# Kernel optimization log

Measured on AMD Instinct MI355X. Metric: run time of the kernel, lower is better.

The kernel has to match this reference:

```python
import jax, jax.numpy as jnp
import numpy as np

D_MODEL = 2048
N_HEADS = 16
HEAD_DIM = D_MODEL // N_HEADS


def setup_inputs() -> dict:
    key = jax.random.key(0)
    k_x, k_wqkv, k_bqkv, k_wo, k_bo = jax.random.split(key, 5)
    B, T = 4, 1024
    s_in = 1.0 / np.sqrt(D_MODEL)
    return {
        "x": jax.random.normal(k_x, (B, T, D_MODEL), dtype=jnp.float32),
        "w_qkv": jax.random.uniform(k_wqkv, (D_MODEL, 3 * D_MODEL), jnp.float32, -s_in, s_in),
        "b_qkv": jax.random.uniform(k_bqkv, (3 * D_MODEL,), jnp.float32, -s_in, s_in),
        "w_out": jax.random.uniform(k_wo, (D_MODEL, D_MODEL), jnp.float32, -s_in, s_in),
        "b_out": jax.random.uniform(k_bo, (D_MODEL,), jnp.float32, -s_in, s_in),
    }


def reference(x, w_qkv, b_qkv, w_out, b_out) -> jnp.ndarray:
    B, T, C = x.shape
    qkv = x @ w_qkv + b_qkv                      # [B, T, 3C]
    q, k, v = jnp.split(qkv, 3, axis=-1)
    # [B, H, T, Dh]
    q = q.reshape(B, T, N_HEADS, HEAD_DIM).transpose(0, 2, 1, 3)
    k = k.reshape(B, T, N_HEADS, HEAD_DIM).transpose(0, 2, 1, 3)
    v = v.reshape(B, T, N_HEADS, HEAD_DIM).transpose(0, 2, 1, 3)
    scale = 1.0 / np.sqrt(HEAD_DIM).astype(np.float32)
    att = jnp.einsum("bhqd,bhkd->bhqk", q, k) * scale   # [B, H, T, T]
    causal = jnp.tril(jnp.ones((T, T), dtype=bool))
    att = jnp.where(causal, att, -jnp.inf)
    att = jax.nn.softmax(att, axis=-1)
    out = jnp.einsum("bhqk,bhkd->bhqd", att, v)          # [B, H, T, Dh]
    out = out.transpose(0, 2, 1, 3).reshape(B, T, C)
    return out @ w_out + b_out
```

## Files before the change

kernel.cpp:

```cpp
#include <hip/hip_runtime.h>
#include <hip/hip_bf16.h>
#include <math.h>

#define DM    2048
#define DQKV  6144
#define NH    16
#define DH    128
#define TT    1024
#define BB    4

typedef __bf16 bf16_t;
typedef __bf16 bf16x4 __attribute__((ext_vector_type(4)));
typedef __bf16 bf16x8 __attribute__((ext_vector_type(8)));
typedef float  f32x4  __attribute__((ext_vector_type(4)));

__device__ __forceinline__ void async16(const void* g, void* lds) {
  __builtin_amdgcn_global_load_lds(
      (const __attribute__((address_space(1))) unsigned int*)g,
      (__attribute__((address_space(3))) unsigned int*)lds, 16, 0, 0);
}

__device__ __forceinline__ void block_barrier() {
  asm volatile("" ::: "memory");
  __builtin_amdgcn_s_barrier();
  asm volatile("" ::: "memory");
}

__global__ __launch_bounds__(256) void prep_kernel(
    const float* __restrict__ x, bf16_t* __restrict__ xb,
    const float* __restrict__ w_qkv, bf16_t* __restrict__ wqkv_t,
    const float* __restrict__ w_out, bf16_t* __restrict__ wout_t) {
  const int tid = threadIdx.x;
  const int bx = blockIdx.x;
  if (bx < 4096) {
    const size_t i = ((size_t)bx * 256 + tid) * 8;
    float4 a = *(const float4*)(x + i);
    float4 b = *(const float4*)(x + i + 4);
    bf16x8 o = {(bf16_t)a.x, (bf16_t)a.y, (bf16_t)a.z, (bf16_t)a.w,
                (bf16_t)b.x, (bf16_t)b.y, (bf16_t)b.z, (bf16_t)b.w};
    *(bf16x8*)(xb + i) = o;
    return;
  }
  __shared__ bf16_t tile[64][72];
  const float* W;
  bf16_t* Wt;
  int K, N, tn, tk;
  if (bx < 7168) {
    const int t = bx - 4096;
    W = w_qkv; Wt = wqkv_t; K = 2048; N = 6144;
    tn = (t % 96) * 64; tk = (t / 96) * 64;
  } else {
    const int t = bx - 7168;
    W = w_out; Wt = wout_t; K = 2048; N = 2048;
    tn = (t % 32) * 64; tk = (t / 32) * 64;
  }
  {
    int r = tid >> 2, c0 = (tid & 3) * 16;
    const float* src = W + (size_t)(tk + r) * N + tn + c0;
#pragma unroll
    for (int j = 0; j < 4; ++j) {
      float4 v = *(const float4*)(src + j * 4);
      tile[r][c0 + j * 4 + 0] = (bf16_t)v.x;
      tile[r][c0 + j * 4 + 1] = (bf16_t)v.y;
      tile[r][c0 + j * 4 + 2] = (bf16_t)v.z;
      tile[r][c0 + j * 4 + 3] = (bf16_t)v.w;
    }
  }
  __syncthreads();
  {
    int n = tid >> 2, c0 = (tid & 3) * 16;
    bf16_t* dst = Wt + (size_t)(tn + n) * K + tk + c0;
#pragma unroll
    for (int j = 0; j < 4; ++j) {
      bf16x4 t = {tile[c0 + j * 4 + 0][n], tile[c0 + j * 4 + 1][n],
                  tile[c0 + j * 4 + 2][n], tile[c0 + j * 4 + 3][n]};
      *(bf16x4*)(dst + j * 4) = t;
    }
  }
}

__global__ __launch_bounds__(256) void v_transpose_kernel(
    const bf16_t* __restrict__ qkv, bf16_t* __restrict__ Vt_g) {
  __shared__ bf16_t tile[64][72];
  const int tid = threadIdx.x;
  const int dt = blockIdx.x;
  const int tt = blockIdx.y;
  const int bh = blockIdx.z;
  const int b = bh >> 4, h = bh & 15;
  {
    int r = tid >> 2, c0 = (tid & 3) * 16;
    const bf16_t* src =
        qkv + (size_t)(b * TT + tt * 64 + r) * DQKV + 2 * DM + h * DH + dt * 64 + c0;
    *(bf16x8*)&tile[r][c0]     = *(const bf16x8*)(src);
    *(bf16x8*)&tile[r][c0 + 8] = *(const bf16x8*)(src + 8);
  }
  __syncthreads();
  {
    int n = tid >> 2, c0 = (tid & 3) * 16;
    bf16_t* dst = Vt_g + (size_t)(bh * DH + dt * 64 + n) * TT + tt * 64 + c0;
#pragma unroll
    for (int j = 0; j < 4; ++j) {
      bf16x4 t = {tile[c0 + j * 4 + 0][n], tile[c0 + j * 4 + 1][n],
                  tile[c0 + j * 4 + 2][n], tile[c0 + j * 4 + 3][n]};
      *(bf16x4*)(dst + j * 4) = t;
    }
  }
}

template <bool OUT_BF16, int BCH, bool WRITE_VT>
__global__ __launch_bounds__(512, 2) void gemm_big_kernel(
    const bf16_t* __restrict__ A, const bf16_t* __restrict__ Bt,
    const float* __restrict__ bias, void* __restrict__ out,
    bf16_t* __restrict__ vt, int M, int N, int K, int nbm) {
  __shared__ __align__(16) bf16_t As[2][256 * 64];
  __shared__ __align__(16) bf16_t Bs[2][BCH * 64 * 64];

  const int tid  = threadIdx.x;
  const int lane = tid & 63;
  const int wave = tid >> 6;
  const int ln   = lane & 15;
  const int quad = lane >> 4;

  const int cpx = gridDim.x >> 3;
  const int wg  = (blockIdx.x & 7) * cpx + (blockIdx.x >> 3);
  const int bm  = wg & (nbm - 1);
  const int bn  = wg / nbm;

  const bf16_t* Abase = A + (size_t)bm * 256 * K;
  const bf16_t* Bbase = Bt + (size_t)bn * (BCH * 64) * K;

  const int m0 = (wave >> 2) * 128;
  const int n0 = (wave & 3) * (BCH * 16);

  f32x4 acc[8][BCH] = {};

  const int NT = K >> 6;

  auto stageA = [&](int kt, int d) {
#pragma unroll
    for (int s = 0; s < 4; ++s) {
      const int fb  = s * 512 + wave * 64;
      const int f   = fb + lane;
      const int row = f >> 3, c = f & 7;
      const int gc  = c ^ (row & 7);
      async16(Abase + (size_t)row * K + kt * 64 + gc * 8,
              (char*)(&As[d][0]) + fb * 16);
    }
  };
  auto stageB = [&](int kt, int d) {
#pragma unroll
    for (int s = 0; s < BCH; ++s) {
      const int fb  = s * 512 + wave * 64;
      const int f   = fb + lane;
      const int row = f >> 3, c = f & 7;
      const int gc  = c ^ (row & 7);
      async16(Bbase + (size_t)row * K + kt * 64 + gc * 8,
              (char*)(&Bs[d][0]) + fb * 16);
    }
  };
  auto vm_lpt = [&] {
    if constexpr (BCH == 3)
      asm volatile("s_waitcnt vmcnt(7)" ::: "memory");
    else
      asm volatile("s_waitcnt vmcnt(6)" ::: "memory");
  };

  stageA(0, 0);
  stageB(0, 0);
  stageA(1, 1);
  stageB(1, 1);
  vm_lpt();
  block_barrier();

  for (int kt = 0; kt < NT; ++kt) {
    const int cur = kt & 1;

    bf16x8 af[8][2], bfr[BCH][2];
#pragma unroll
    for (int ks = 0; ks < 2; ++ks) {
#pragma unroll
      for (int i = 0; i < 8; ++i) {
        const int row = m0 + 16 * i + ln;
        const int c = (ks * 4 + quad) ^ (row & 7);
        af[i][ks] =
            *(const bf16x8*)((const char*)(&As[cur][0]) + ((row * 8 + c) << 4));
      }
#pragma unroll
      for (int j = 0; j < BCH; ++j) {
        const int row = n0 + 16 * j + ln;
        const int c = (ks * 4 + quad) ^ (row & 7);
        bfr[j][ks] =
            *(const bf16x8*)((const char*)(&Bs[cur][0]) + ((row * 8 + c) << 4));
      }
    }
    asm volatile("s_waitcnt lgkmcnt(0)" ::: "memory");
    block_barrier();

    if (kt + 2 < NT) stageA(kt + 2, cur);
    __builtin_amdgcn_s_setprio(1);
#pragma unroll
    for (int i = 0; i < 8; ++i)
#pragma unroll
      for (int j = 0; j < BCH; ++j)
        acc[i][j] = __builtin_amdgcn_mfma_f32_16x16x32_bf16(af[i][0], bfr[j][0],
                                                            acc[i][j], 0, 0, 0);
    __builtin_amdgcn_s_setprio(0);
    if (kt + 2 < NT) stageB(kt + 2, cur);
    __builtin_amdgcn_s_setprio(1);
#pragma unroll
    for (int i = 0; i < 8; ++i)
#pragma unroll
      for (int j = 0; j < BCH; ++j)
        acc[i][j] = __builtin_amdgcn_mfma_f32_16x16x32_bf16(af[i][1], bfr[j][1],
                                                            acc[i][j], 0, 0, 0);
    __builtin_amdgcn_s_setprio(0);

    if (kt + 2 < NT)
      vm_lpt();
    else
      asm volatile("s_waitcnt vmcnt(0)" ::: "memory");
    block_barrier();
  }

#pragma unroll
  for (int i = 0; i < 8; ++i) {
    const int rowg = bm * 256 + m0 + 16 * i + quad * 4;
#pragma unroll
    for (int j = 0; j < BCH; ++j) {
      const int cb   = bn * (BCH * 64) + n0 + 16 * j;
      const int colg = cb + ln;
      const float bb = bias[colg];
      if (WRITE_VT && cb >= 2 * DM) {
        const int vrow = ((rowg >> 10) << 11) + (colg - 2 * DM);
        bf16x4 v = {(bf16_t)(acc[i][j][0] + bb), (bf16_t)(acc[i][j][1] + bb),
                    (bf16_t)(acc[i][j][2] + bb), (bf16_t)(acc[i][j][3] + bb)};
        *(bf16x4*)(vt + (size_t)vrow * TT + (rowg & (TT - 1))) = v;
      } else {
#pragma unroll
        for (int r = 0; r < 4; ++r) {
          float val = acc[i][j][r] + bb;
          if (OUT_BF16)
            ((bf16_t*)out)[(size_t)(rowg + r) * N + colg] = (bf16_t)val;
          else
            ((float*)out)[(size_t)(rowg + r) * N + colg] = val;
        }
      }
    }
  }
}

__global__ __launch_bounds__(256, 2) void attn_kernel(
    const bf16_t* __restrict__ qkv, const bf16_t* __restrict__ Vt_g,
    bf16_t* __restrict__ attout) {
  const int bx = blockIdx.x;
  const int bh = bx & 63;
  const int j_  = bx >> 6;
  const int rr  = j_ >> 2, cc_ = j_ & 3;
  const int qt  = (rr & 1) ? (rr * 4 + (3 - cc_)) : (rr * 4 + cc_);
  const int b  = bh >> 4;
  const int h  = bh & 15;
  const int tid  = threadIdx.x;
  const int lane = tid & 63;
  const int wave = tid >> 6;
  const int ln   = lane & 15;
  const int quad = lane >> 4;

  __shared__ __align__(16) bf16_t Ks[2][64 * 128];
  __shared__ __align__(16) bf16_t Vs[2][128 * 64];
  __shared__ __align__(16) bf16_t Ps[4 * 16 * 64];

  const float scale = 0.08838834764831845f;
  const float SHIFT = 12.0f;
  const int q0 = qt * 64 + wave * 16;

  bf16x8 aq[4];
  {
    const bf16_t* qrow = qkv + (size_t)(b * TT + q0 + ln) * DQKV + h * DH;
#pragma unroll
    for (int kt = 0; kt < 4; ++kt)
      aq[kt] = *(const bf16x8*)(qrow + kt * 32 + quad * 8);
  }

  auto stage = [&](int c, int buf) {
    const int kc = c * 64;
#pragma unroll
    for (int j = 0; j < 4; ++j) {
      const int fb = j * 256 + wave * 64;
      const int l  = fb + lane;
      {
        const int row = l >> 4, cc = l & 15;
        const int gc  = cc ^ (row & 7);
        const bf16_t* g =
            qkv + (size_t)(b * TT + kc + row) * DQKV + DM + h * DH + gc * 8;
        async16(g, (char*)(&Ks[buf][0]) + fb * 16);
      }
      {
        const int d = l >> 3, cc = l & 7;
        const int gc = cc ^ (d & 7);
        const bf16_t* g = Vt_g + (size_t)(bh * DH + d) * TT + kc + gc * 8;
        async16(g, (char*)(&Vs[buf][0]) + fb * 16);
      }
    }
  };

  f32x4 o[8] = {};
  float lp[4] = {0.f, 0.f, 0.f, 0.f};

  stage(0, 0);

  for (int c = 0; c <= qt; ++c) {
    const int cur = c & 1;
    const char* Kc = (const char*)(&Ks[cur][0]);
    const char* Vc = (const char*)(&Vs[cur][0]);

    asm volatile("s_waitcnt lgkmcnt(0)" ::: "memory");
    block_barrier();
    if (c < qt) {
      stage(c + 1, cur ^ 1);
      asm volatile("s_waitcnt vmcnt(8)" ::: "memory");
    } else {
      asm volatile("s_waitcnt vmcnt(0)" ::: "memory");
    }
    block_barrier();

    f32x4 sacc[4];
    __builtin_amdgcn_s_setprio(1);
#pragma unroll
    for (int jt = 0; jt < 4; ++jt) {
      sacc[jt] = (f32x4){0.f, 0.f, 0.f, 0.f};
#pragma unroll
      for (int kt = 0; kt < 4; ++kt) {
        const int row = jt * 16 + ln;
        const int sc  = (kt * 4 + quad) ^ (row & 7);
        bf16x8 bk = *(const bf16x8*)(Kc + row * 256 + sc * 16);
        sacc[jt] = __builtin_amdgcn_mfma_f32_16x16x32_bf16(aq[kt], bk,
                                                           sacc[jt], 0, 0, 0);
      }
    }
    __builtin_amdgcn_s_setprio(0);

    const int kc = c * 64;
    const bool diag = (c == qt);
#pragma unroll
    for (int jt = 0; jt < 4; ++jt) {
      const int colg = kc + jt * 16 + ln;
#pragma unroll
      for (int r = 0; r < 4; ++r) {
        float sv = sacc[jt][r] * scale - SHIFT;
        if (diag && colg > q0 + quad * 4 + r) sv = -1e30f;
        float pv = __expf(sv);
        lp[r] += pv;
        const int row = quad * 4 + r;
        const int col = jt * 16 + ln;
        const int sc  = (col >> 3) ^ (row & 7);
        Ps[wave * 1024 + row * 64 + sc * 8 + (col & 7)] = (bf16_t)pv;
      }
    }

    __builtin_amdgcn_s_setprio(1);
#pragma unroll
    for (int ks = 0; ks < 2; ++ks) {
      const int psc = (ks * 4 + quad) ^ (ln & 7);
      bf16x8 ap =
          *(const bf16x8*)((const char*)Ps + wave * 2048 + ln * 128 + psc * 16);
#pragma unroll
      for (int nt = 0; nt < 8; ++nt) {
        const int row = nt * 16 + ln;
        const int sc  = (ks * 4 + quad) ^ (row & 7);
        bf16x8 bv = *(const bf16x8*)(Vc + row * 128 + sc * 16);
        o[nt] = __builtin_amdgcn_mfma_f32_16x16x32_bf16(ap, bv, o[nt], 0, 0, 0);
      }
    }
    __builtin_amdgcn_s_setprio(0);
  }

#pragma unroll
  for (int off = 1; off < 16; off <<= 1)
#pragma unroll
    for (int r = 0; r < 4; ++r) lp[r] += __shfl_xor(lp[r], off, 64);

#pragma unroll
  for (int r = 0; r < 4; ++r) {
    float inv = 1.0f / lp[r];
    int t = q0 + quad * 4 + r;
    bf16_t* orow = attout + (size_t)(b * TT + t) * DM + h * DH;
#pragma unroll
    for (int nt = 0; nt < 8; ++nt)
      orow[nt * 16 + ln] = (bf16_t)(o[nt][r] * inv);
  }
}

extern "C" void kernel_launch(void* const* d_in, const int* in_sizes, int n_in,
                              void* d_out, int out_size, void* d_ws,
                              size_t ws_size, hipStream_t stream) {
  const float* x     = (const float*)d_in[0];
  const float* w_qkv = (const float*)d_in[1];
  const float* b_qkv = (const float*)d_in[2];
  const float* w_out = (const float*)d_in[3];
  const float* b_out = (const float*)d_in[4];
  float* out = (float*)d_out;

  char* ws = (char*)d_ws;
  bf16_t* qkv    = (bf16_t*)(ws);
  bf16_t* wqkv_t = (bf16_t*)(ws + 50331648);
  bf16_t* wout_t = (bf16_t*)(ws + 75497472);
  bf16_t* xb     = (bf16_t*)(ws + 83886080);
  bf16_t* attout = xb;

  const bool fuse_vt = (ws_size >= 117440512);
  bf16_t* Vt_g = fuse_vt ? (bf16_t*)(ws + 100663296) : wqkv_t;

  prep_kernel<<<dim3(8192), dim3(256), 0, stream>>>(x, xb, w_qkv, wqkv_t,
                                                    w_out, wout_t);
  if (fuse_vt) {
    gemm_big_kernel<true, 3, true><<<dim3(512), dim3(512), 0, stream>>>(
        xb, wqkv_t, b_qkv, qkv, Vt_g, 4096, 6144, 2048, 16);
  } else {
    gemm_big_kernel<true, 3, false><<<dim3(512), dim3(512), 0, stream>>>(
        xb, wqkv_t, b_qkv, qkv, nullptr, 4096, 6144, 2048, 16);
    v_transpose_kernel<<<dim3(2, 16, 64), dim3(256), 0, stream>>>(qkv, Vt_g);
  }
  attn_kernel<<<dim3(1024), dim3(256), 0, stream>>>(qkv, Vt_g, attout);
  gemm_big_kernel<false, 2, false><<<dim3(256), dim3(512), 0, stream>>>(
      attout, wout_t, b_out, out, nullptr, 4096, 2048, 2048, 16);
}
```

Before: 329.9 us.

## Restructure GEMM main loop into quadrant-ordered MFMA phases with split A prefetch

The main loop of the bf16 GEMM now loads A and B fragments from LDS in four smaller quadrant phases instead of loading all of them up front. Each phase's MFMAs run as soon as its fragments arrive, and B fragments are reused across phases, which cuts register pressure and overlaps LDS reads with matrix math. The A tile's global-to-LDS staging is split in two. Half of the next tile is prefetched into the idle buffer while the current tile is being computed, and the other half plus B is issued after the barrier, with adjusted vmcnt waits. The aim is to hide memory latency better and lower VGPR use, at the cost of tricky wait-count accounting and more phase boundaries.

Result: slower. 361.8 us (+9.7%).

```diff
diff --git a/kernel.cpp b/kernel.cpp
--- a/kernel.cpp
+++ b/kernel.cpp
@@ -136,88 +136,134 @@
 
   const int NT = K >> 6;
 
-  auto stageA = [&](int kt, int d) {
-#pragma unroll
-    for (int s = 0; s < 4; ++s) {
-      const int fb  = s * 512 + wave * 64;
-      const int f   = fb + lane;
-      const int row = f >> 3, c = f & 7;
-      const int gc  = c ^ (row & 7);
-      async16(Abase + (size_t)row * K + kt * 64 + gc * 8,
-              (char*)(&As[d][0]) + fb * 16);
-    }
+  auto sA = [&](int kt, int d, int s) {
+    const int fb  = s * 512 + wave * 64;
+    const int f   = fb + lane;
+    const int row = f >> 3, c = f & 7;
+    const int gc  = c ^ (row & 7);
+    async16(Abase + (size_t)row * K + kt * 64 + gc * 8,
+            (char*)(&As[d][0]) + fb * 16);
   };
-  auto stageB = [&](int kt, int d) {
-#pragma unroll
-    for (int s = 0; s < BCH; ++s) {
-      const int fb  = s * 512 + wave * 64;
-      const int f   = fb + lane;
-      const int row = f >> 3, c = f & 7;
-      const int gc  = c ^ (row & 7);
-      async16(Bbase + (size_t)row * K + kt * 64 + gc * 8,
-              (char*)(&Bs[d][0]) + fb * 16);
-    }
+  auto sB = [&](int kt, int d, int s) {
+    const int fb  = s * 512 + wave * 64;
+    const int f   = fb + lane;
+    const int row = f >> 3, c = f & 7;
+    const int gc  = c ^ (row & 7);
+    async16(Bbase + (size_t)row * K + kt * 64 + gc * 8,
+            (char*)(&Bs[d][0]) + fb * 16);
   };
-  auto vm_lpt = [&] {
+  auto vm_steady = [&] {
     if constexpr (BCH == 3)
-      asm volatile("s_waitcnt vmcnt(7)" ::: "memory");
+      asm volatile("s_waitcnt vmcnt(5)" ::: "memory");
     else
-      asm volatile("s_waitcnt vmcnt(6)" ::: "memory");
+      asm volatile("s_waitcnt vmcnt(4)" ::: "memory");
   };
 
-  stageA(0, 0);
-  stageB(0, 0);
-  stageA(1, 1);
-  stageB(1, 1);
-  vm_lpt();
+#pragma unroll
+  for (int s = 0; s < 4; ++s) sA(0, 0, s);
+#pragma unroll
+  for (int s = 0; s < BCH; ++s) sB(0, 0, s);
+  sA(1, 1, 1);
+  sA(1, 1, 3);
+#pragma unroll
+  for (int s = 0; s < BCH; ++s) sB(1, 1, s);
+  vm_steady();
   block_barrier();
 
   for (int kt = 0; kt < NT; ++kt) {
     const int cur = kt & 1;
-
-    bf16x8 af[8][2], bfr[BCH][2];
-#pragma unroll
-    for (int ks = 0; ks < 2; ++ks) {
-#pragma unroll
-      for (int i = 0; i < 8; ++i) {
-        const int row = m0 + 16 * i + ln;
-        const int c = (ks * 4 + quad) ^ (row & 7);
-        af[i][ks] =
-            *(const bf16x8*)((const char*)(&As[cur][0]) + ((row * 8 + c) << 4));
-      }
-#pragma unroll
-      for (int j = 0; j < BCH; ++j) {
-        const int row = n0 + 16 * j + ln;
-        const int c = (ks * 4 + quad) ^ (row & 7);
-        bfr[j][ks] =
-            *(const bf16x8*)((const char*)(&Bs[cur][0]) + ((row * 8 + c) << 4));
-      }
-    }
+    const char* cA = (const char*)(&As[cur][0]);
+    const char* cB = (const char*)(&Bs[cur][0]);
+    bf16x8 a[4], brg[BCH];
+
+#pragma unroll
+    for (int i = 0; i < 4; ++i) {
+      const int row = m0 + 16 * i + ln;
+      const int c = quad ^ (row & 7);
+      a[i] = *(const bf16x8*)(cA + ((row * 8 + c) << 4));
+    }
+#pragma unroll
+    for (int j = 0; j < BCH; ++j) {
+      const int row = n0 + 16 * j + ln;
+      const int c = quad ^ (row & 7);
+      brg[j] = *(const bf16x8*)(cB + ((row * 8 + c) << 4));
+    }
+    if (kt + 1 < NT) {
+      sA(kt + 1, cur ^ 1, 0);
+      sA(kt + 1, cur ^ 1, 2);
+    }
+    __builtin_amdgcn_s_setprio(1);
+#pragma unroll
+    for (int i = 0; i < 4; ++i)
+#pragma unroll
+      for (int j = 0; j < BCH; ++j)
+        acc[i][j] = __builtin_amdgcn_mfma_f32_16x16x32_bf16(a[i], brg[j],
+                                                            acc[i][j], 0, 0, 0);
+    __builtin_amdgcn_s_setprio(0);
+
+#pragma unroll
+    for (int i = 0; i < 4; ++i) {
+      const int row = m0 + 64 + 16 * i + ln;
+      const int c = quad ^ (row & 7);
+      a[i] = *(const bf16x8*)(cA + ((row * 8 + c) << 4));
+    }
+    __builtin_amdgcn_s_setprio(1);
+#pragma unroll
+    for (int i = 0; i < 4; ++i)
+#pragma unroll
+      for (int j = 0; j < BCH; ++j)
+        acc[4 + i][j] = __builtin_amdgcn_mfma_f32_16x16x32_bf16(
+            a[i], brg[j], acc[4 + i][j], 0, 0, 0);
+    __builtin_amdgcn_s_setprio(0);
+
+#pragma unroll
+    for (int i = 0; i < 4; ++i) {
+      const int row = m0 + 64 + 16 * i + ln;
+      const int c = (4 + quad) ^ (row & 7);
+      a[i] = *(const bf16x8*)(cA + ((row * 8 + c) << 4));
+    }
+#pragma unroll
+    for (int j = 0; j < BCH; ++j) {
+      const int row = n0 + 16 * j + ln;
+      const int c = (4 + quad) ^ (row & 7);
+      brg[j] = *(const bf16x8*)(cB + ((row * 8 + c) << 4));
+    }
+    __builtin_amdgcn_s_setprio(1);
+#pragma unroll
+    for (int i = 0; i < 4; ++i)
+#pragma unroll
+      for (int j = 0; j < BCH; ++j)
+        acc[4 + i][j] = __builtin_amdgcn_mfma_f32_16x16x32_bf16(
+            a[i], brg[j], acc[4 + i][j], 0, 0, 0);
+    __builtin_amdgcn_s_setprio(0);
+
+#pragma unroll
+    for (int i = 0; i < 4; ++i) {
+      const int row = m0 + 16 * i + ln;
+      const int c = (4 + quad) ^ (row & 7);
+      a[i] = *(const bf16x8*)(cA + ((row * 8 + c) << 4));
+    }
+    __builtin_amdgcn_s_setprio(1);
+#pragma unroll
+    for (int i = 0; i < 4; ++i)
+#pragma unroll
+      for (int j = 0; j < BCH; ++j)
+        acc[i][j] = __builtin_amdgcn_mfma_f32_16x16x32_bf16(a[i], brg[j],
+                                                            acc[i][j], 0, 0, 0);
+    __builtin_amdgcn_s_setprio(0);
+
     asm volatile("s_waitcnt lgkmcnt(0)" ::: "memory");
     block_barrier();
 
-    if (kt + 2 < NT) stageA(kt + 2, cur);
-    __builtin_amdgcn_s_setprio(1);
-#pragma unroll
-    for (int i = 0; i < 8; ++i)
-#pragma unroll
-      for (int j = 0; j < BCH; ++j)
-        acc[i][j] = __builtin_amdgcn_mfma_f32_16x16x32_bf16(af[i][0], bfr[j][0],
-                                                            acc[i][j], 0, 0, 0);
-    __builtin_amdgcn_s_setprio(0);
-    if (kt + 2 < NT) stageB(kt + 2, cur);
-    __builtin_amdgcn_s_setprio(1);
-#pragma unroll
-    for (int i = 0; i < 8; ++i)
-#pragma unroll
-      for (int j = 0; j < BCH; ++j)
-        acc[i][j] = __builtin_amdgcn_mfma_f32_16x16x32_bf16(af[i][1], bfr[j][1],
-                                                            acc[i][j], 0, 0, 0);
-    __builtin_amdgcn_s_setprio(0);
-
+    if (kt + 2 < NT) {
+      sA(kt + 2, cur, 1);
+      sA(kt + 2, cur, 3);
+#pragma unroll
+      for (int s = 0; s < BCH; ++s) sB(kt + 2, cur, s);
+    }
     if (kt + 2 < NT)
-      vm_lpt();
-    else
+      vm_steady();
+    else if (kt == NT - 2)
       asm volatile("s_waitcnt vmcnt(0)" ::: "memory");
     block_barrier();
   }
```

## Add 128x128-tile double-buffered GEMM for output projection and vectorize weight transpose

Applied to the files above, without the earlier changes.

Replaces the output projection GEMM with a new 128x128-tile kernel using 256 threads, two blocks per CU, double-buffered async global-to-LDS loads with XOR swizzle, and MFMA interleaved with staging of the next tiles. This doubles the grid from 256 to 512 workgroups so more of the GPU's CUs get work for the 4096x2048 output. The prep transpose also writes LDS with 4-wide vector stores and writes global memory with 8-wide stores. The smaller tiles mean less reuse per loaded byte, and the output stores remain scalar fp32.

After: 318.8 us. 1.03x faster.

```diff
diff --git a/kernel.cpp b/kernel.cpp
--- a/kernel.cpp
+++ b/kernel.cpp
@@ -60,22 +60,22 @@
 #pragma unroll
     for (int j = 0; j < 4; ++j) {
       float4 v = *(const float4*)(src + j * 4);
-      tile[r][c0 + j * 4 + 0] = (bf16_t)v.x;
-      tile[r][c0 + j * 4 + 1] = (bf16_t)v.y;
-      tile[r][c0 + j * 4 + 2] = (bf16_t)v.z;
-      tile[r][c0 + j * 4 + 3] = (bf16_t)v.w;
+      bf16x4 t = {(bf16_t)v.x, (bf16_t)v.y, (bf16_t)v.z, (bf16_t)v.w};
+      *(bf16x4*)&tile[r][c0 + j * 4] = t;
     }
   }
   __syncthreads();
   {
     int n = tid >> 2, c0 = (tid & 3) * 16;
     bf16_t* dst = Wt + (size_t)(tn + n) * K + tk + c0;
-#pragma unroll
-    for (int j = 0; j < 4; ++j) {
-      bf16x4 t = {tile[c0 + j * 4 + 0][n], tile[c0 + j * 4 + 1][n],
-                  tile[c0 + j * 4 + 2][n], tile[c0 + j * 4 + 3][n]};
-      *(bf16x4*)(dst + j * 4) = t;
-    }
+    bf16x8 t0 = {tile[c0 + 0][n], tile[c0 + 1][n], tile[c0 + 2][n],
+                 tile[c0 + 3][n], tile[c0 + 4][n], tile[c0 + 5][n],
+                 tile[c0 + 6][n], tile[c0 + 7][n]};
+    bf16x8 t1 = {tile[c0 + 8][n],  tile[c0 + 9][n],  tile[c0 + 10][n],
+                 tile[c0 + 11][n], tile[c0 + 12][n], tile[c0 + 13][n],
+                 tile[c0 + 14][n], tile[c0 + 15][n]};
+    *(bf16x8*)(dst) = t0;
+    *(bf16x8*)(dst + 8) = t1;
   }
 }
 
@@ -245,6 +245,128 @@
             ((float*)out)[(size_t)(rowg + r) * N + colg] = val;
         }
       }
+    }
+  }
+}
+
+__global__ __launch_bounds__(256, 2) void gemm128_kernel(
+    const bf16_t* __restrict__ A, const bf16_t* __restrict__ Bt,
+    const float* __restrict__ bias, float* __restrict__ out,
+    int M, int N, int K, int nbm) {
+  __shared__ __align__(16) bf16_t As[2][128 * 64];
+  __shared__ __align__(16) bf16_t Bs[2][128 * 64];
+
+  const int tid  = threadIdx.x;
+  const int lane = tid & 63;
+  const int wave = tid >> 6;
+  const int ln   = lane & 15;
+  const int quad = lane >> 4;
+
+  const int cpx = gridDim.x >> 3;
+  const int wg  = (blockIdx.x & 7) * cpx + (blockIdx.x >> 3);
+  const int bm  = wg & (nbm - 1);
+  const int bn  = wg / nbm;
+
+  const bf16_t* Abase = A + (size_t)bm * 128 * K;
+  const bf16_t* Bbase = Bt + (size_t)bn * 128 * K;
+
+  const int m0 = (wave >> 1) * 64;
+  const int n0 = (wave & 1) * 64;
+
+  f32x4 acc[4][4] = {};
+
+  const int NT = K >> 6;
+
+  auto stageA = [&](int kt, int d) {
+#pragma unroll
+    for (int s = 0; s < 4; ++s) {
+      const int fb  = s * 256 + wave * 64;
+      const int f   = fb + lane;
+      const int row = f >> 3, c = f & 7;
+      const int gc  = c ^ (row & 7);
+      async16(Abase + (size_t)row * K + kt * 64 + gc * 8,
+              (char*)(&As[d][0]) + fb * 16);
+    }
+  };
+  auto stageB = [&](int kt, int d) {
+#pragma unroll
+    for (int s = 0; s < 4; ++s) {
+      const int fb  = s * 256 + wave * 64;
+      const int f   = fb + lane;
+      const int row = f >> 3, c = f & 7;
+      const int gc  = c ^ (row & 7);
+      async16(Bbase + (size_t)row * K + kt * 64 + gc * 8,
+              (char*)(&Bs[d][0]) + fb * 16);
+    }
+  };
+
+  stageA(0, 0);
+  stageB(0, 0);
+  stageA(1, 1);
+  stageB(1, 1);
+  asm volatile("s_waitcnt vmcnt(8)" ::: "memory");
+  block_barrier();
+
+  for (int kt = 0; kt < NT; ++kt) {
+    const int cur = kt & 1;
+
+    bf16x8 af[4][2], bfr[4][2];
+#pragma unroll
+    for (int ks = 0; ks < 2; ++ks) {
+#pragma unroll
+      for (int i = 0; i < 4; ++i) {
+        const int row = m0 + 16 * i + ln;
+        const int c = (ks * 4 + quad) ^ (row & 7);
+        af[i][ks] =
+            *(const bf16x8*)((const char*)(&As[cur][0]) + ((row * 8 + c) << 4));
+      }
+#pragma unroll
+      for (int j = 0; j < 4; ++j) {
+        const int row = n0 + 16 * j + ln;
+        const int c = (ks * 4 + quad) ^ (row & 7);
+        bfr[j][ks] =
+            *(const bf16x8*)((const char*)(&Bs[cur][0]) + ((row * 8 + c) << 4));
+      }
+    }
+    asm volatile("s_waitcnt lgkmcnt(0)" ::: "memory");
+    block_barrier();
+
+    if (kt + 2 < NT) stageA(kt + 2, cur);
+    __builtin_amdgcn_s_setprio(1);
+#pragma unroll
+    for (int i = 0; i < 4; ++i)
+#pragma unroll
+      for (int j = 0; j < 4; ++j)
+        acc[i][j] = __builtin_amdgcn_mfma_f32_16x16x32_bf16(af[i][0], bfr[j][0],
+                                                            acc[i][j], 0, 0, 0);
+    __builtin_amdgcn_s_setprio(0);
+    if (kt + 2 < NT) stageB(kt + 2, cur);
+    __builtin_amdgcn_s_setprio(1);
+#pragma unroll
+    for (int i = 0; i < 4; ++i)
+#pragma unroll
+      for (int j = 0; j < 4; ++j)
+        acc[i][j] = __builtin_amdgcn_mfma_f32_16x16x32_bf16(af[i][1], bfr[j][1],
+                                                            acc[i][j], 0, 0, 0);
+    __builtin_amdgcn_s_setprio(0);
+
+    if (kt + 2 < NT)
+      asm volatile("s_waitcnt vmcnt(8)" ::: "memory");
+    else
+      asm volatile("s_waitcnt vmcnt(0)" ::: "memory");
+    block_barrier();
+  }
+
+#pragma unroll
+  for (int i = 0; i < 4; ++i) {
+    const int rowg = bm * 128 + m0 + 16 * i + quad * 4;
+#pragma unroll
+    for (int j = 0; j < 4; ++j) {
+      const int colg = bn * 128 + n0 + 16 * j + ln;
+      const float bb = bias[colg];
+#pragma unroll
+      for (int r = 0; r < 4; ++r)
+        out[(size_t)(rowg + r) * N + colg] = acc[i][j][r] + bb;
     }
   }
 }
@@ -421,6 +543,6 @@
     v_transpose_kernel<<<dim3(2, 16, 64), dim3(256), 0, stream>>>(qkv, Vt_g);
   }
   attn_kernel<<<dim3(1024), dim3(256), 0, stream>>>(qkv, Vt_g, attout);
-  gemm_big_kernel<false, 2, false><<<dim3(256), dim3(512), 0, stream>>>(
-      attout, wout_t, b_out, out, nullptr, 4096, 2048, 2048, 16);
-}
+  gemm128_kernel<<<dim3(512), dim3(256), 0, stream>>>(
+      attout, wout_t, b_out, out, 4096, 2048, 2048, 32);
+}
```
